# Kernel optimization log

Hardware: AMD Instinct MI355X
Metric: run time of the kernel (lower is better)

Reference implementation:

```python
import jax, jax.numpy as jnp
import numpy as np

EMBED = 384
HEAD = 64


def setup_inputs() -> dict:
    key = jax.random.key(0)
    kx, kq, kk, kv = jax.random.split(key, 4)
    B, T = 4, 4096
    x = jax.random.normal(kx, (B, T, EMBED), dtype=jnp.float32)
    # torch Linear(384, 64, bias=False): weight (64, 384), y = x @ W.T.
    # Store pre-transposed as (EMBED, HEAD) so y = x @ W.
    s = 1.0 / np.sqrt(EMBED)  # kaiming-uniform-ish scale
    Wq = jax.random.uniform(kq, (EMBED, HEAD), jnp.float32, -s, s)
    Wk = jax.random.uniform(kk, (EMBED, HEAD), jnp.float32, -s, s)
    Wv = jax.random.uniform(kv, (EMBED, HEAD), jnp.float32, -s, s)
    return {"x": x, "Wq": Wq, "Wk": Wk, "Wv": Wv}


def reference(x, Wq, Wk, Wv):
    # q, k, v: [B, T, H]
    q = x @ Wq
    k = x @ Wk
    v = x @ Wv
    scale = k.shape[-1] ** (-0.5)
    scores = jnp.einsum("bth,bsh->bts", q, k) * scale  # [B, T, T]
    # Faithful to the original: tril, then mask anything equal to 0 with -inf
    # (this also masks exact zeros inside the causal region).
    tril = jnp.tril(scores)
    masked = jnp.where(tril == 0, -jnp.inf, tril)
    attn = jax.nn.softmax(masked, axis=-1)
    out = jnp.einsum("bts,bsh->bth", attn, v)  # [B, T, H]
    return out
```

## Files before the change

### kernel.cpp

```cpp
#include <hip/hip_runtime.h>
#include <hip/hip_bf16.h>
#include <stdint.h>


#define EMBED 384
#define HEAD  64
#define NB    4
#define NT    4096
#define NROWS (NB * NT)
#define NSPLIT 4

#define SCALE_Q 0.18033688011112042f

typedef short bf16x8 __attribute__((ext_vector_type(8)));
typedef float f32x4  __attribute__((ext_vector_type(4)));

__device__ __forceinline__ unsigned short bfround(float f) {
    union { float f; unsigned u; } v; v.f = f;
    return (unsigned short)((v.u + 0x8000u) >> 16);
}
__device__ __forceinline__ unsigned packbf(float lo, float hi) {
    union { float f; unsigned u; } a, b; a.f = lo; b.f = hi;
    return ((a.u + 0x8000u) >> 16) | ((b.u + 0x8000u) & 0xFFFF0000u);
}
__device__ __forceinline__ unsigned cvtpk(float lo, float hi) {
    unsigned r;
    asm("v_cvt_pk_bf16_f32 %0, %1, %2" : "=v"(r) : "v"(lo), "v"(hi));
    return r;
}

__device__ __forceinline__ void pl_swap32(unsigned& a, unsigned& b) {
    asm("v_permlane32_swap_b32 %0, %1" : "+v"(a), "+v"(b));
}
__device__ __forceinline__ void pl_swap16(unsigned& a, unsigned& b) {
    asm("v_permlane16_swap_b32 %0, %1" : "+v"(a), "+v"(b));
}

__global__ __launch_bounds__(256)
void wprep_kernel(const float* __restrict__ Wq,
                  const float* __restrict__ Wk,
                  const float* __restrict__ Wv,
                  unsigned short* __restrict__ Wt)
{
    int idx = blockIdx.x * 256 + threadIdx.x;
    int k = idx / 192;
    int n = idx - k * 192;
    int sel = n >> 6, nc = n & 63;
    const float* wp = (sel == 0) ? Wq : ((sel == 1) ? Wk : Wv);
    Wt[n * EMBED + k] = bfround(wp[(size_t)k * HEAD + nc]);
}

__global__ __launch_bounds__(512)
void proj_kernel(const float* __restrict__ x,
                 const unsigned short* __restrict__ Wt,
                 unsigned short* __restrict__ Qo,
                 unsigned short* __restrict__ Ko,
                 unsigned short* __restrict__ Vto)
{
    __shared__ __attribute__((aligned(16))) unsigned short ws[2][192][128];
    __shared__ __attribute__((aligned(16))) unsigned short xs[2][64][128];
    unsigned short (*vbuf)[72] = (unsigned short (*)[72])&xs[1][0][0];

    const int t    = threadIdx.x;
    const int lane = t & 63;
    const int w    = t >> 6;
    const int quad = lane >> 4;
    const int l16  = lane & 15;
    const int wr   = w & 3;
    const int wc   = w >> 2;
    const int r0   = blockIdx.x * 64;

    const int xr  = t >> 5, xc4 = t & 31;
    const int xch = xc4 >> 1, xsub = (xc4 & 1) * 4;
    const int wrw = t >> 4, wcc = t & 15;

    f32x4 acc[6];
#pragma unroll
    for (int i = 0; i < 6; ++i) acc[i] = (f32x4){0.f, 0.f, 0.f, 0.f};

    float4 xv[4];
    uint4  wv[6];
#pragma unroll
    for (int i = 0; i < 4; ++i)
        xv[i] = *(const float4*)(x + (size_t)(r0 + xr + 16 * i) * EMBED + xc4 * 4);
#pragma unroll
    for (int i = 0; i < 6; ++i)
        wv[i] = *(const uint4*)(Wt + (size_t)(wrw + 32 * i) * EMBED + wcc * 8);

    int cur = 0;
#pragma unroll
    for (int ph = 0; ph < 3; ++ph) {
#pragma unroll
        for (int i = 0; i < 4; ++i) {
            int row = xr + 16 * i;
            uint2 pw; pw.x = packbf(xv[i].x, xv[i].y); pw.y = packbf(xv[i].z, xv[i].w);
            *(uint2*)&xs[cur][row][((xch ^ (row & 15)) << 3) + xsub] = pw;
        }
#pragma unroll
        for (int i = 0; i < 6; ++i) {
            int row = wrw + 32 * i;
            *(uint4*)&ws[cur][row][(wcc ^ (row & 15)) << 3] = wv[i];
        }
        __syncthreads();

        if (ph < 2) {
            const int k0 = (ph + 1) * 128;
#pragma unroll
            for (int i = 0; i < 4; ++i)
                xv[i] = *(const float4*)(x + (size_t)(r0 + xr + 16 * i) * EMBED + k0 + xc4 * 4);
#pragma unroll
            for (int i = 0; i < 6; ++i)
                wv[i] = *(const uint4*)(Wt + (size_t)(wrw + 32 * i) * EMBED + k0 + wcc * 8);
        }

#pragma unroll
        for (int s = 0; s < 4; ++s) {
            bf16x8 a = *(const bf16x8*)&xs[cur][wr * 16 + l16][((s * 4 + quad) ^ l16) << 3];
#pragma unroll
            for (int ng = 0; ng < 6; ++ng) {
                bf16x8 b = *(const bf16x8*)&ws[cur][wc * 96 + ng * 16 + l16][((s * 4 + quad) ^ l16) << 3];
                acc[ng] = __builtin_amdgcn_mfma_f32_16x16x32_bf16(a, b, acc[ng], 0, 0, 0);
            }
        }
        cur ^= 1;
    }
    __syncthreads();

#pragma unroll
    for (int ng = 0; ng < 6; ++ng) {
        int cg = wc * 96 + ng * 16 + l16;
#pragma unroll
        for (int r = 0; r < 4; ++r) {
            int row = r0 + wr * 16 + quad * 4 + r;
            float vv = acc[ng][r];
            if (cg < 64) {
                Qo[(size_t)row * HEAD + cg] = bfround(vv * SCALE_Q);
            } else if (cg < 128) {
                Ko[(size_t)row * HEAD + (cg - 64)] = bfround(vv);
            } else {
                vbuf[cg - 128][wr * 16 + quad * 4 + r] = bfround(vv);
            }
        }
    }
    __syncthreads();
    {
        const int batch = r0 >> 12;
        const int s0 = r0 & (NT - 1);
        const int d = t >> 3, c = t & 7;
        *(uint4*)(Vto + ((size_t)(batch * HEAD + d)) * NT + s0 + c * 8) =
            *(const uint4*)&vbuf[d][c * 8];
    }
}

__global__ __launch_bounds__(512, 8)
void attn_kernel(const unsigned short* __restrict__ Qi,
                 const unsigned short* __restrict__ Ki,
                 const unsigned short* __restrict__ Vti,
                 float* __restrict__ opart,
                 float* __restrict__ lpart)
{
    __shared__ __attribute__((aligned(16))) unsigned short Kt[2][64][64];
    __shared__ __attribute__((aligned(16))) unsigned short Vs[2][64][64];

    const int t    = threadIdx.x;
    const int w    = t >> 6;
    const int lane = t & 63;
    const int quad = lane >> 4;
    const int l16  = lane & 15;
    const int qg   = w >> 1;
    const int sh   = w & 1;

    const int u = blockIdx.x;
    const int g = u >> 4;
    const int m = (g < 32) ? (63 - g) : (g - 32);
    const int sp = (u >> 2) & 3;
    const int batch = u & 3;
    const int ntiles = (m >= sp) ? (((m - sp) >> 2) + 1) : 0;
    const int q0 = m * 64 + qg * 16;

    const unsigned short* Kbg = Ki  + (size_t)batch * NT * HEAD;
    const unsigned short* Vbg = Vti + (size_t)batch * HEAD * NT;

    bf16x8 bq0, bq1;
    {
        const unsigned short* qp = Qi + (size_t)(batch * NT + q0 + l16) * HEAD + quad * 8;
        bq0 = *(const bf16x8*)(qp);
        bq1 = *(const bf16x8*)(qp + 32);
    }

    f32x4 o[4];
#pragma unroll
    for (int i = 0; i < 4; ++i) o[i] = (f32x4){0.f, 0.f, 0.f, 0.f};
    float rs = 0.f;

    const int srow = t >> 3, sc = t & 7;
    const int scc  = sc ^ (srow & 7);
    const int sw   = l16 & 7;

    uint4 kr, vr;
    if (ntiles > 0) {
        kr = *(const uint4*)(Kbg + (size_t)(sp * 64 + srow) * HEAD + sc * 8);
        vr = *(const uint4*)(Vbg + (size_t)srow * NT + sp * 64 + sc * 8);
    }

    int cur = 0;
    for (int j = 0; j < ntiles; ++j) {
        const int kt = sp + 4 * j;
        *(uint4*)&Kt[cur][srow][scc * 8] = kr;
        *(uint4*)&Vs[cur][srow][scc * 8] = vr;
        __syncthreads();

        if (j + 1 < ntiles) {
            const int ktn = kt + 4;
            kr = *(const uint4*)(Kbg + (size_t)(ktn * 64 + srow) * HEAD + sc * 8);
            vr = *(const uint4*)(Vbg + (size_t)srow * NT + ktn * 64 + sc * 8);
        }

        const bool diag = (kt == m);
        uint2 pw[2];
#pragma unroll
        for (int tsl = 0; tsl < 2; ++tsl) {
            const int ts = sh * 2 + tsl;
            bf16x8 ak0 = *(const bf16x8*)&Kt[cur][ts * 16 + l16][(quad ^ sw) * 8];
            bf16x8 ak1 = *(const bf16x8*)&Kt[cur][ts * 16 + l16][((4 + quad) ^ sw) * 8];
            f32x4 z = (f32x4){0.f, 0.f, 0.f, 0.f};
            z = __builtin_amdgcn_mfma_f32_16x16x32_bf16(ak0, bq0, z, 0, 0, 0);
            z = __builtin_amdgcn_mfma_f32_16x16x32_bf16(ak1, bq1, z, 0, 0, 0);
            float p[4];
#pragma unroll
            for (int r = 0; r < 4; ++r) {
                float pv = __builtin_amdgcn_exp2f(z[r]);
                if (diag) {
                    int sg = kt * 64 + ts * 16 + quad * 4 + r;
                    pv = (sg > q0 + l16) ? 0.f : pv;
                }
                p[r] = pv;
            }
            rs += (p[0] + p[1]) + (p[2] + p[3]);
            pw[tsl].x = cvtpk(p[0], p[1]);
            pw[tsl].y = cvtpk(p[2], p[3]);
        }

        unsigned a0 = pw[0].x, c0 = pw[0].y, b0 = pw[1].x, d0 = pw[1].y;
        pl_swap32(a0, b0); pl_swap32(c0, d0);
        pl_swap16(a0, b0); pl_swap16(c0, d0);
        union { unsigned uu[4]; bf16x8 v; } ua;
        ua.uu[0] = a0; ua.uu[1] = c0; ua.uu[2] = b0; ua.uu[3] = d0;
        const bf16x8 ap = ua.v;

#pragma unroll
        for (int nd = 0; nd < 4; ++nd) {
            bf16x8 av = *(const bf16x8*)&Vs[cur][nd * 16 + l16][((4 * sh + quad) ^ sw) * 8];
            o[nd] = __builtin_amdgcn_mfma_f32_16x16x32_bf16(ap, av, o[nd], 0, 0, 0);
        }
        cur ^= 1;
    }

    rs += __shfl_xor(rs, 16, 64);
    rs += __shfl_xor(rs, 32, 64);

    __syncthreads();
    float* osc = (float*)&Kt[0][0][0];
    float* rsc = (float*)&Vs[0][0][0];
    if (sh == 1) {
#pragma unroll
        for (int nd = 0; nd < 4; ++nd)
#pragma unroll
            for (int r = 0; r < 4; ++r)
                osc[(qg * 16 + quad * 4 + r) * 64 + nd * 16 + l16] = o[nd][r];
        if (quad == 0) rsc[qg * 16 + l16] = rs;
    }
    __syncthreads();
    if (sh == 0) {
        rs += rsc[qg * 16 + l16];
        if (quad == 0)
            lpart[(size_t)sp * NROWS + batch * NT + q0 + l16] = rs;
        float* ob = opart + (size_t)sp * NROWS * HEAD;
#pragma unroll
        for (int r = 0; r < 4; ++r) {
            size_t off = (size_t)(batch * NT + q0 + quad * 4 + r) * HEAD;
#pragma unroll
            for (int nd = 0; nd < 4; ++nd)
                ob[off + nd * 16 + l16] =
                    o[nd][r] + osc[(qg * 16 + quad * 4 + r) * 64 + nd * 16 + l16];
        }
    }
}

__global__ __launch_bounds__(256)
void combine_kernel(const float* __restrict__ opart,
                    const float* __restrict__ lpart,
                    float* __restrict__ out)
{
    int gid = blockIdx.x * 256 + threadIdx.x;
    int row = gid >> 4;
    int d4  = (gid & 15) * 4;
    const size_t st = (size_t)NROWS * HEAD;
    const float* p0 = opart + (size_t)row * HEAD + d4;
    f32x4 a = *(const f32x4*)(p0);
    f32x4 b = *(const f32x4*)(p0 + st);
    f32x4 c = *(const f32x4*)(p0 + 2 * st);
    f32x4 d = *(const f32x4*)(p0 + 3 * st);
    float inv = 1.0f / (lpart[row] + lpart[NROWS + row] +
                        lpart[2 * NROWS + row] + lpart[3 * NROWS + row]);
    f32x4 res = (a + b) + (c + d);
    res[0] *= inv; res[1] *= inv; res[2] *= inv; res[3] *= inv;
    *(f32x4*)(out + (size_t)row * HEAD + d4) = res;
}

extern "C" void kernel_launch(void* const* d_in, const int* in_sizes, int n_in,
                              void* d_out, int out_size, void* d_ws, size_t ws_size,
                              hipStream_t stream)
{
    const float* x  = (const float*)d_in[0];
    const float* Wq = (const float*)d_in[1];
    const float* Wk = (const float*)d_in[2];
    const float* Wv = (const float*)d_in[3];
    float* out = (float*)d_out;

    unsigned short* Qw  = (unsigned short*)d_ws;
    unsigned short* Kw  = Qw + (size_t)NROWS * HEAD;
    unsigned short* Vtw = Kw + (size_t)NROWS * HEAD;
    unsigned short* Wtw = Vtw + (size_t)NROWS * HEAD;
    float* opart = (float*)(Wtw + (size_t)192 * EMBED);
    float* lpart = opart + (size_t)NSPLIT * NROWS * HEAD;

    wprep_kernel<<<(192 * EMBED) / 256, 256, 0, stream>>>(Wq, Wk, Wv, Wtw);
    proj_kernel<<<256, 512, 0, stream>>>(x, Wtw, Qw, Kw, Vtw);
    attn_kernel<<<1024, 512, 0, stream>>>(Qw, Kw, Vtw, opart, lpart);
    combine_kernel<<<NROWS * 16 / 256, 256, 0, stream>>>(opart, lpart, out);
}
```

Before: 103.8 us.

## Pair long and short causal query tiles per block to balance work

Each attention block now handles two query tiles, m=63-p and m=p, one after the other within one loop, so every block does about the same amount of causal work. The grid is halved to 512 blocks. A merge step between the two phases writes out the first tile's partial results. The aim is to remove load imbalance and the tail of short blocks. In exchange it adds an extra barrier and merge mid-loop, a dedicated osc shared buffer that raises LDS use, and lower launch-bounds occupancy (4 instead of 8).

```diff
diff --git a/kernel.cpp b/kernel.cpp
--- a/kernel.cpp
+++ b/kernel.cpp
@@ -152,7 +152,7 @@
     }
 }
 
-__global__ __launch_bounds__(512, 8)
+__global__ __launch_bounds__(512, 4)
 void attn_kernel(const unsigned short* __restrict__ Qi,
                  const unsigned short* __restrict__ Ki,
                  const unsigned short* __restrict__ Vti,
@@ -161,6 +161,8 @@
 {
     __shared__ __attribute__((aligned(16))) unsigned short Kt[2][64][64];
     __shared__ __attribute__((aligned(16))) unsigned short Vs[2][64][64];
+    __shared__ __attribute__((aligned(16))) float osc[64][64];
+    __shared__ float rsc[64];
 
     const int t    = threadIdx.x;
     const int w    = t >> 6;
@@ -171,19 +173,24 @@
     const int sh   = w & 1;
 
     const int u = blockIdx.x;
-    const int g = u >> 4;
-    const int m = (g < 32) ? (63 - g) : (g - 32);
+    const int batch = u & 3;
     const int sp = (u >> 2) & 3;
-    const int batch = u & 3;
-    const int ntiles = (m >= sp) ? (((m - sp) >> 2) + 1) : 0;
-    const int q0 = m * 64 + qg * 16;
+    const int p  = u >> 4;
+    const int mA = 63 - p;
+    const int mB = p;
+    const int nA = ((mA - sp) >> 2) + 1;
+    const int nB = (mB >= sp) ? (((mB - sp) >> 2) + 1) : 0;
+    const int jtot = nA + nB;
 
     const unsigned short* Kbg = Ki  + (size_t)batch * NT * HEAD;
     const unsigned short* Vbg = Vti + (size_t)batch * HEAD * NT;
-
+    const unsigned short* Qb  = Qi  + (size_t)batch * NT * HEAD;
+
+    int mcur = mA;
+    int q0 = mA * 64 + qg * 16;
     bf16x8 bq0, bq1;
     {
-        const unsigned short* qp = Qi + (size_t)(batch * NT + q0 + l16) * HEAD + quad * 8;
+        const unsigned short* qp = Qb + (size_t)(q0 + l16) * HEAD + quad * 8;
         bq0 = *(const bf16x8*)(qp);
         bq1 = *(const bf16x8*)(qp + 32);
     }
@@ -197,26 +204,69 @@
     const int scc  = sc ^ (srow & 7);
     const int sw   = l16 & 7;
 
+    auto merge_out = [&](int mm) {
+        float r = rs;
+        r += __shfl_xor(r, 16, 64);
+        r += __shfl_xor(r, 32, 64);
+        if (sh == 1) {
+#pragma unroll
+            for (int nd = 0; nd < 4; ++nd)
+#pragma unroll
+                for (int rr = 0; rr < 4; ++rr)
+                    osc[qg * 16 + quad * 4 + rr][nd * 16 + l16] = o[nd][rr];
+            if (quad == 0) rsc[qg * 16 + l16] = r;
+        }
+        __syncthreads();
+        if (sh == 0) {
+            const int qq0 = mm * 64 + qg * 16;
+            r += rsc[qg * 16 + l16];
+            if (quad == 0)
+                lpart[(size_t)sp * NROWS + batch * NT + qq0 + l16] = r;
+            float* ob = opart + (size_t)sp * NROWS * HEAD;
+#pragma unroll
+            for (int rr = 0; rr < 4; ++rr) {
+                size_t off = (size_t)(batch * NT + qq0 + quad * 4 + rr) * HEAD;
+#pragma unroll
+                for (int nd = 0; nd < 4; ++nd)
+                    ob[off + nd * 16 + l16] =
+                        o[nd][rr] + osc[qg * 16 + quad * 4 + rr][nd * 16 + l16];
+            }
+        }
+    };
+
     uint4 kr, vr;
-    if (ntiles > 0) {
+    {
         kr = *(const uint4*)(Kbg + (size_t)(sp * 64 + srow) * HEAD + sc * 8);
         vr = *(const uint4*)(Vbg + (size_t)srow * NT + sp * 64 + sc * 8);
     }
 
     int cur = 0;
-    for (int j = 0; j < ntiles; ++j) {
-        const int kt = sp + 4 * j;
+    for (int j = 0; j < jtot; ++j) {
+        const bool phB = (j >= nA);
+        const int kt = sp + 4 * (phB ? (j - nA) : j);
         *(uint4*)&Kt[cur][srow][scc * 8] = kr;
         *(uint4*)&Vs[cur][srow][scc * 8] = vr;
         __syncthreads();
 
-        if (j + 1 < ntiles) {
-            const int ktn = kt + 4;
+        if (j == nA) {
+            merge_out(mA);
+#pragma unroll
+            for (int i = 0; i < 4; ++i) o[i] = (f32x4){0.f, 0.f, 0.f, 0.f};
+            rs = 0.f;
+            mcur = mB;
+            q0 = mB * 64 + qg * 16;
+            const unsigned short* qp = Qb + (size_t)(q0 + l16) * HEAD + quad * 8;
+            bq0 = *(const bf16x8*)(qp);
+            bq1 = *(const bf16x8*)(qp + 32);
+        }
+
+        if (j + 1 < jtot) {
+            const int ktn = sp + 4 * ((j + 1 >= nA) ? (j + 1 - nA) : (j + 1));
             kr = *(const uint4*)(Kbg + (size_t)(ktn * 64 + srow) * HEAD + sc * 8);
             vr = *(const uint4*)(Vbg + (size_t)srow * NT + ktn * 64 + sc * 8);
         }
 
-        const bool diag = (kt == m);
+        const bool diag = (kt == mcur);
         uint2 pw[2];
 #pragma unroll
         for (int tsl = 0; tsl < 2; ++tsl) {
@@ -226,7 +276,7 @@
             f32x4 z = (f32x4){0.f, 0.f, 0.f, 0.f};
             z = __builtin_amdgcn_mfma_f32_16x16x32_bf16(ak0, bq0, z, 0, 0, 0);
             z = __builtin_amdgcn_mfma_f32_16x16x32_bf16(ak1, bq1, z, 0, 0, 0);
-            float p[4];
+            float pq[4];
 #pragma unroll
             for (int r = 0; r < 4; ++r) {
                 float pv = __builtin_amdgcn_exp2f(z[r]);
@@ -234,11 +284,11 @@
                     int sg = kt * 64 + ts * 16 + quad * 4 + r;
                     pv = (sg > q0 + l16) ? 0.f : pv;
                 }
-                p[r] = pv;
+                pq[r] = pv;
             }
-            rs += (p[0] + p[1]) + (p[2] + p[3]);
-            pw[tsl].x = cvtpk(p[0], p[1]);
-            pw[tsl].y = cvtpk(p[2], p[3]);
+            rs += (pq[0] + pq[1]) + (pq[2] + pq[3]);
+            pw[tsl].x = cvtpk(pq[0], pq[1]);
+            pw[tsl].y = cvtpk(pq[2], pq[3]);
         }
 
         unsigned a0 = pw[0].x, c0 = pw[0].y, b0 = pw[1].x, d0 = pw[1].y;
@@ -256,33 +306,19 @@
         cur ^= 1;
     }
 
-    rs += __shfl_xor(rs, 16, 64);
-    rs += __shfl_xor(rs, 32, 64);
-
-    __syncthreads();
-    float* osc = (float*)&Kt[0][0][0];
-    float* rsc = (float*)&Vs[0][0][0];
-    if (sh == 1) {
-#pragma unroll
-        for (int nd = 0; nd < 4; ++nd)
-#pragma unroll
-            for (int r = 0; r < 4; ++r)
-                osc[(qg * 16 + quad * 4 + r) * 64 + nd * 16 + l16] = o[nd][r];
-        if (quad == 0) rsc[qg * 16 + l16] = rs;
-    }
-    __syncthreads();
-    if (sh == 0) {
-        rs += rsc[qg * 16 + l16];
+    merge_out(nB > 0 ? mB : mA);
+
+    if (nB == 0 && sh == 0) {
+        const int qq0 = mB * 64 + qg * 16;
         if (quad == 0)
-            lpart[(size_t)sp * NROWS + batch * NT + q0 + l16] = rs;
+            lpart[(size_t)sp * NROWS + batch * NT + qq0 + l16] = 0.f;
         float* ob = opart + (size_t)sp * NROWS * HEAD;
 #pragma unroll
-        for (int r = 0; r < 4; ++r) {
-            size_t off = (size_t)(batch * NT + q0 + quad * 4 + r) * HEAD;
+        for (int rr = 0; rr < 4; ++rr) {
+            size_t off = (size_t)(batch * NT + qq0 + quad * 4 + rr) * HEAD;
 #pragma unroll
             for (int nd = 0; nd < 4; ++nd)
-                ob[off + nd * 16 + l16] =
-                    o[nd][r] + osc[(qg * 16 + quad * 4 + r) * 64 + nd * 16 + l16];
+                ob[off + nd * 16 + l16] = 0.f;
         }
     }
 }
@@ -327,6 +363,6 @@
 
     wprep_kernel<<<(192 * EMBED) / 256, 256, 0, stream>>>(Wq, Wk, Wv, Wtw);
     proj_kernel<<<256, 512, 0, stream>>>(x, Wtw, Qw, Kw, Vtw);
-    attn_kernel<<<1024, 512, 0, stream>>>(Qw, Kw, Vtw, opart, lpart);
+    attn_kernel<<<512, 512, 0, stream>>>(Qw, Kw, Vtw, opart, lpart);
     combine_kernel<<<NROWS * 16 / 256, 256, 0, stream>>>(opart, lpart, out);
 }
```

Result: slower. 108.6 us (+4.7%).

## Switch attention kernel to 32x32x16 MFMA with 256-thread blocks

Applied to the files above, without the earlier changes.

Rewrites the attention inner loop around the 32x32x16 bf16 MFMA: each wave now owns 32 queries and 32 keys instead of 16x16 tiles, and the block shrinks from 8 to 4 waves. This means fewer MFMA issues per tile, fewer LDS fragment reads and a simpler permlane shuffle. Each thread now stages two rows of K and V per tile. The epilogue goes through a padded LDS transpose so opart can be written with coalesced vector stores. The larger accumulators raise register pressure, and halving waves per block may reduce latency hiding.

```diff
diff --git a/kernel.cpp b/kernel.cpp
--- a/kernel.cpp
+++ b/kernel.cpp
@@ -14,6 +14,7 @@
 
 typedef short bf16x8 __attribute__((ext_vector_type(8)));
 typedef float f32x4  __attribute__((ext_vector_type(4)));
+typedef float f32x16 __attribute__((ext_vector_type(16)));
 
 __device__ __forceinline__ unsigned short bfround(float f) {
     union { float f; unsigned u; } v; v.f = f;
@@ -28,12 +29,8 @@
     asm("v_cvt_pk_bf16_f32 %0, %1, %2" : "=v"(r) : "v"(lo), "v"(hi));
     return r;
 }
-
 __device__ __forceinline__ void pl_swap32(unsigned& a, unsigned& b) {
     asm("v_permlane32_swap_b32 %0, %1" : "+v"(a), "+v"(b));
-}
-__device__ __forceinline__ void pl_swap16(unsigned& a, unsigned& b) {
-    asm("v_permlane16_swap_b32 %0, %1" : "+v"(a), "+v"(b));
 }
 
 __global__ __launch_bounds__(256)
@@ -152,21 +149,21 @@
     }
 }
 
-__global__ __launch_bounds__(512, 8)
+__global__ __launch_bounds__(256, 4)
 void attn_kernel(const unsigned short* __restrict__ Qi,
                  const unsigned short* __restrict__ Ki,
                  const unsigned short* __restrict__ Vti,
                  float* __restrict__ opart,
                  float* __restrict__ lpart)
 {
-    __shared__ __attribute__((aligned(16))) unsigned short Kt[2][64][64];
-    __shared__ __attribute__((aligned(16))) unsigned short Vs[2][64][64];
+    __shared__ __attribute__((aligned(16))) unsigned short KV[2][2][64][64];
+    __shared__ float rsc[64];
 
     const int t    = threadIdx.x;
     const int w    = t >> 6;
     const int lane = t & 63;
-    const int quad = lane >> 4;
-    const int l16  = lane & 15;
+    const int l32  = lane & 31;
+    const int hi   = lane >> 5;
     const int qg   = w >> 1;
     const int sh   = w & 1;
 
@@ -176,113 +173,137 @@
     const int sp = (u >> 2) & 3;
     const int batch = u & 3;
     const int ntiles = (m >= sp) ? (((m - sp) >> 2) + 1) : 0;
-    const int q0 = m * 64 + qg * 16;
+    const int q0w = m * 64 + qg * 32;
 
     const unsigned short* Kbg = Ki  + (size_t)batch * NT * HEAD;
     const unsigned short* Vbg = Vti + (size_t)batch * HEAD * NT;
 
-    bf16x8 bq0, bq1;
-    {
-        const unsigned short* qp = Qi + (size_t)(batch * NT + q0 + l16) * HEAD + quad * 8;
-        bq0 = *(const bf16x8*)(qp);
-        bq1 = *(const bf16x8*)(qp + 32);
-    }
-
-    f32x4 o[4];
-#pragma unroll
-    for (int i = 0; i < 4; ++i) o[i] = (f32x4){0.f, 0.f, 0.f, 0.f};
+    bf16x8 bq[4];
+#pragma unroll
+    for (int dc = 0; dc < 4; ++dc)
+        bq[dc] = *(const bf16x8*)(Qi + (size_t)(batch * NT + q0w + l32) * HEAD
+                                  + dc * 16 + hi * 8);
+
+    f32x16 o0, o1;
+#pragma unroll
+    for (int i = 0; i < 16; ++i) { o0[i] = 0.f; o1[i] = 0.f; }
     float rs = 0.f;
 
-    const int srow = t >> 3, sc = t & 7;
-    const int scc  = sc ^ (srow & 7);
-    const int sw   = l16 & 7;
-
-    uint4 kr, vr;
+    const int srow0 = t >> 3, sc = t & 7;
+    const int srow1 = srow0 + 32;
+    const int scc0 = sc ^ (srow0 & 7);
+    const int scc1 = sc ^ (srow1 & 7);
+    const int r7 = l32 & 7;
+
+    uint4 kr0, kr1, vr0, vr1;
     if (ntiles > 0) {
-        kr = *(const uint4*)(Kbg + (size_t)(sp * 64 + srow) * HEAD + sc * 8);
-        vr = *(const uint4*)(Vbg + (size_t)srow * NT + sp * 64 + sc * 8);
+        kr0 = *(const uint4*)(Kbg + (size_t)(sp * 64 + srow0) * HEAD + sc * 8);
+        kr1 = *(const uint4*)(Kbg + (size_t)(sp * 64 + srow1) * HEAD + sc * 8);
+        vr0 = *(const uint4*)(Vbg + (size_t)srow0 * NT + sp * 64 + sc * 8);
+        vr1 = *(const uint4*)(Vbg + (size_t)srow1 * NT + sp * 64 + sc * 8);
     }
 
     int cur = 0;
     for (int j = 0; j < ntiles; ++j) {
         const int kt = sp + 4 * j;
-        *(uint4*)&Kt[cur][srow][scc * 8] = kr;
-        *(uint4*)&Vs[cur][srow][scc * 8] = vr;
+        *(uint4*)&KV[cur][0][srow0][scc0 * 8] = kr0;
+        *(uint4*)&KV[cur][0][srow1][scc1 * 8] = kr1;
+        *(uint4*)&KV[cur][1][srow0][scc0 * 8] = vr0;
+        *(uint4*)&KV[cur][1][srow1][scc1 * 8] = vr1;
         __syncthreads();
 
         if (j + 1 < ntiles) {
             const int ktn = kt + 4;
-            kr = *(const uint4*)(Kbg + (size_t)(ktn * 64 + srow) * HEAD + sc * 8);
-            vr = *(const uint4*)(Vbg + (size_t)srow * NT + ktn * 64 + sc * 8);
+            kr0 = *(const uint4*)(Kbg + (size_t)(ktn * 64 + srow0) * HEAD + sc * 8);
+            kr1 = *(const uint4*)(Kbg + (size_t)(ktn * 64 + srow1) * HEAD + sc * 8);
+            vr0 = *(const uint4*)(Vbg + (size_t)srow0 * NT + ktn * 64 + sc * 8);
+            vr1 = *(const uint4*)(Vbg + (size_t)srow1 * NT + ktn * 64 + sc * 8);
+        }
+
+        f32x16 z;
+#pragma unroll
+        for (int i = 0; i < 16; ++i) z[i] = 0.f;
+        const unsigned short* kb = &KV[cur][0][sh * 32 + l32][0];
+#pragma unroll
+        for (int dc = 0; dc < 4; ++dc) {
+            bf16x8 ak = *(const bf16x8*)&kb[(((dc << 1) | hi) ^ r7) << 3];
+            z = __builtin_amdgcn_mfma_f32_32x32x16_bf16(ak, bq[dc], z, 0, 0, 0);
         }
 
         const bool diag = (kt == m);
-        uint2 pw[2];
-#pragma unroll
-        for (int tsl = 0; tsl < 2; ++tsl) {
-            const int ts = sh * 2 + tsl;
-            bf16x8 ak0 = *(const bf16x8*)&Kt[cur][ts * 16 + l16][(quad ^ sw) * 8];
-            bf16x8 ak1 = *(const bf16x8*)&Kt[cur][ts * 16 + l16][((4 + quad) ^ sw) * 8];
-            f32x4 z = (f32x4){0.f, 0.f, 0.f, 0.f};
-            z = __builtin_amdgcn_mfma_f32_16x16x32_bf16(ak0, bq0, z, 0, 0, 0);
-            z = __builtin_amdgcn_mfma_f32_16x16x32_bf16(ak1, bq1, z, 0, 0, 0);
-            float p[4];
-#pragma unroll
-            for (int r = 0; r < 4; ++r) {
-                float pv = __builtin_amdgcn_exp2f(z[r]);
-                if (diag) {
-                    int sg = kt * 64 + ts * 16 + quad * 4 + r;
-                    pv = (sg > q0 + l16) ? 0.f : pv;
-                }
-                p[r] = pv;
+        const int qglob = q0w + l32;
+        float pq[16];
+#pragma unroll
+        for (int r = 0; r < 16; ++r) {
+            float pv = __builtin_amdgcn_exp2f(z[r]);
+            if (diag) {
+                int sg = kt * 64 + sh * 32 + (r & 3) + 8 * (r >> 2) + 4 * hi;
+                pv = (sg > qglob) ? 0.f : pv;
             }
-            rs += (p[0] + p[1]) + (p[2] + p[3]);
-            pw[tsl].x = cvtpk(p[0], p[1]);
-            pw[tsl].y = cvtpk(p[2], p[3]);
-        }
-
-        unsigned a0 = pw[0].x, c0 = pw[0].y, b0 = pw[1].x, d0 = pw[1].y;
-        pl_swap32(a0, b0); pl_swap32(c0, d0);
-        pl_swap16(a0, b0); pl_swap16(c0, d0);
-        union { unsigned uu[4]; bf16x8 v; } ua;
-        ua.uu[0] = a0; ua.uu[1] = c0; ua.uu[2] = b0; ua.uu[3] = d0;
-        const bf16x8 ap = ua.v;
-
-#pragma unroll
-        for (int nd = 0; nd < 4; ++nd) {
-            bf16x8 av = *(const bf16x8*)&Vs[cur][nd * 16 + l16][((4 * sh + quad) ^ sw) * 8];
-            o[nd] = __builtin_amdgcn_mfma_f32_16x16x32_bf16(ap, av, o[nd], 0, 0, 0);
+            pq[r] = pv;
+        }
+        rs += (((pq[0] + pq[1]) + (pq[2] + pq[3])) + ((pq[4] + pq[5]) + (pq[6] + pq[7])))
+            + (((pq[8] + pq[9]) + (pq[10] + pq[11])) + ((pq[12] + pq[13]) + (pq[14] + pq[15])));
+
+        unsigned x0 = cvtpk(pq[0], pq[1]),  x1 = cvtpk(pq[2], pq[3]);
+        unsigned x2 = cvtpk(pq[4], pq[5]),  x3 = cvtpk(pq[6], pq[7]);
+        unsigned x4 = cvtpk(pq[8], pq[9]),  x5 = cvtpk(pq[10], pq[11]);
+        unsigned x6 = cvtpk(pq[12], pq[13]), x7 = cvtpk(pq[14], pq[15]);
+        pl_swap32(x0, x2); pl_swap32(x1, x3);
+        pl_swap32(x4, x6); pl_swap32(x5, x7);
+        union { unsigned uu[4]; bf16x8 v; } b0, b1;
+        b0.uu[0] = x0; b0.uu[1] = x1; b0.uu[2] = x2; b0.uu[3] = x3;
+        b1.uu[0] = x4; b1.uu[1] = x5; b1.uu[2] = x6; b1.uu[3] = x7;
+
+        const unsigned short* vb0 = &KV[cur][1][l32][0];
+        const unsigned short* vb1 = &KV[cur][1][32 + l32][0];
+#pragma unroll
+        for (int sk = 0; sk < 2; ++sk) {
+            const int c = sh * 4 + sk * 2 + hi;
+            bf16x8 av0 = *(const bf16x8*)&vb0[((c ^ r7) << 3)];
+            bf16x8 av1 = *(const bf16x8*)&vb1[((c ^ r7) << 3)];
+            const bf16x8 bp = sk ? b1.v : b0.v;
+            o0 = __builtin_amdgcn_mfma_f32_32x32x16_bf16(av0, bp, o0, 0, 0, 0);
+            o1 = __builtin_amdgcn_mfma_f32_32x32x16_bf16(av1, bp, o1, 0, 0, 0);
         }
         cur ^= 1;
     }
 
-    rs += __shfl_xor(rs, 16, 64);
-    rs += __shfl_xor(rs, 32, 64);
-
-    __syncthreads();
-    float* osc = (float*)&Kt[0][0][0];
-    float* rsc = (float*)&Vs[0][0][0];
+    float rs2 = rs + __shfl_xor(rs, 32, 64);
+    __syncthreads();
+    float (*osc)[65] = (float (*)[65])&KV[0][0][0][0];
     if (sh == 1) {
 #pragma unroll
-        for (int nd = 0; nd < 4; ++nd)
-#pragma unroll
-            for (int r = 0; r < 4; ++r)
-                osc[(qg * 16 + quad * 4 + r) * 64 + nd * 16 + l16] = o[nd][r];
-        if (quad == 0) rsc[qg * 16 + l16] = rs;
+        for (int r = 0; r < 16; ++r) {
+            osc[(r & 3) + 8 * (r >> 2) + 4 * hi][qg * 32 + l32] = o0[r];
+            osc[32 + (r & 3) + 8 * (r >> 2) + 4 * hi][qg * 32 + l32] = o1[r];
+        }
+        if (lane < 32) rsc[qg * 32 + l32] = rs2;
     }
     __syncthreads();
     if (sh == 0) {
-        rs += rsc[qg * 16 + l16];
-        if (quad == 0)
-            lpart[(size_t)sp * NROWS + batch * NT + q0 + l16] = rs;
-        float* ob = opart + (size_t)sp * NROWS * HEAD;
-#pragma unroll
-        for (int r = 0; r < 4; ++r) {
-            size_t off = (size_t)(batch * NT + q0 + quad * 4 + r) * HEAD;
-#pragma unroll
-            for (int nd = 0; nd < 4; ++nd)
-                ob[off + nd * 16 + l16] =
-                    o[nd][r] + osc[(qg * 16 + quad * 4 + r) * 64 + nd * 16 + l16];
+#pragma unroll
+        for (int r = 0; r < 16; ++r) {
+            osc[(r & 3) + 8 * (r >> 2) + 4 * hi][qg * 32 + l32] += o0[r];
+            osc[32 + (r & 3) + 8 * (r >> 2) + 4 * hi][qg * 32 + l32] += o1[r];
+        }
+        if (lane < 32) {
+            float rtot = rs2 + rsc[qg * 32 + l32];
+            lpart[(size_t)sp * NROWS + batch * NT + m * 64 + qg * 32 + l32] = rtot;
+        }
+    }
+    __syncthreads();
+    {
+        float* ob = opart + (size_t)sp * NROWS * HEAD
+                  + (size_t)(batch * NT + m * 64) * HEAD;
+        const int d0 = (t & 15) * 4;
+#pragma unroll
+        for (int i = 0; i < 4; ++i) {
+            const int q = i * 16 + (t >> 4);
+            f32x4 v;
+            v[0] = osc[d0 + 0][q]; v[1] = osc[d0 + 1][q];
+            v[2] = osc[d0 + 2][q]; v[3] = osc[d0 + 3][q];
+            *(f32x4*)&ob[(size_t)q * HEAD + d0] = v;
         }
     }
 }
@@ -327,6 +348,6 @@
 
     wprep_kernel<<<(192 * EMBED) / 256, 256, 0, stream>>>(Wq, Wk, Wv, Wtw);
     proj_kernel<<<256, 512, 0, stream>>>(x, Wtw, Qw, Kw, Vtw);
-    attn_kernel<<<1024, 512, 0, stream>>>(Qw, Kw, Vtw, opart, lpart);
+    attn_kernel<<<1024, 256, 0, stream>>>(Qw, Kw, Vtw, opart, lpart);
     combine_kernel<<<NROWS * 16 / 256, 256, 0, stream>>>(opart, lpart, out);
 }
```

Measured after the change: 104.8 us. No clear change (+1.0%).
